# Optimization experiments

Hardware: AMD Instinct MI355X
Metric: run time of the kernel (lower is better)

The kernel has to match this reference:

```python
import jax, jax.numpy as jnp
import numpy as np

N_NODES = 20000
N_EDGES = 320000
DIM_IN = 768
DIM_H = 512
S_HOPS = 3
NUM_GNNS = 4
NEG_SLOPE = 0.2  # DGL GATConv default


def setup_inputs() -> dict:
    key = jax.random.key(0)
    ks = jax.random.split(key, 12)
    feat = jax.random.normal(ks[0], (N_NODES, DIM_IN), dtype=jnp.float32)
    src = jax.random.randint(ks[1], (N_EDGES,), 0, N_NODES)
    dst = jax.random.randint(ks[2], (N_EDGES,), 0, N_NODES)
    # learned params
    fc_W = jax.random.normal(ks[3], (DIM_IN, DIM_H), dtype=jnp.float32) * 0.02
    fc_b = jnp.zeros((DIM_H,), dtype=jnp.float32)
    gat_W = jax.random.normal(ks[4], (NUM_GNNS, DIM_H, DIM_H), dtype=jnp.float32) * 0.02
    gat_al = jax.random.normal(ks[5], (NUM_GNNS, DIM_H), dtype=jnp.float32) * 0.1
    gat_ar = jax.random.normal(ks[6], (NUM_GNNS, DIM_H), dtype=jnp.float32) * 0.1
    gat_b = jnp.zeros((NUM_GNNS, DIM_H), dtype=jnp.float32)
    beta = jnp.ones((S_HOPS + 1,), dtype=jnp.float32)
    return {"feat": feat, "fc_W": fc_W, "fc_b": fc_b, "gat_W": gat_W,
            "gat_al": gat_al, "gat_ar": gat_ar, "gat_b": gat_b,
            "beta": beta, "src": src, "dst": dst}


def _gat_layer(h, W, a_l, a_r, b, src, dst):
    z = h @ W                                   # [N, DH]
    el = z @ a_l                                # [N]
    er = z @ a_r                                # [N]
    e = jax.nn.leaky_relu(el[src] + er[dst], NEG_SLOPE)  # [E]
    # edge softmax over incoming edges of each dst node
    m = jax.ops.segment_max(e, dst, num_segments=N_NODES)
    ex = jnp.exp(e - m[dst])
    denom = jax.ops.segment_sum(ex, dst, num_segments=N_NODES)
    alpha = ex / denom[dst]                     # [E]
    out = jax.ops.segment_sum(alpha[:, None] * z[src], dst, num_segments=N_NODES)
    return out + b


def reference(feat, fc_W, fc_b, gat_W, gat_al, gat_ar, gat_b, beta, src, dst):
    h = feat @ fc_W + fc_b                      # dim_in -> 512
    for l in range(NUM_GNNS):
        h = _gat_layer(h, gat_W[l], gat_al[l], gat_ar[l], gat_b[l], src, dst)
    # A_hat = A + I propagation; A_hat @ Z = scatter(Z[src] -> dst) + Z
    Z_prev = h
    Z = beta[0] * Z_prev                        # accumulated Z is computed but the
    for s in range(1, S_HOPS + 1):              # original module returns Z_prev
        Z_s = jax.ops.segment_sum(Z_prev[src], dst, num_segments=N_NODES) + Z_prev
        Z = Z + beta[s] * Z_s
        Z_prev = Z_s
    return Z_prev
```

## Files before the change

kernel.cpp:

```cpp
#include <hip/hip_runtime.h>
#include <math.h>

#define N_NODES 20000
#define M_PAD   20096
#define N_EDGES 320000
#define DIM_IN 768
#define DIM_H 512
#define NUM_GNNS 4
#define NEG_SLOPE 0.2f

typedef __attribute__((ext_vector_type(8))) short short8;
typedef __attribute__((ext_vector_type(4))) float f32x4;

#define GPTR(p) (const __attribute__((address_space(1))) void*)(p)
#define LPTR(p) (__attribute__((address_space(3))) void*)(p)

__device__ __forceinline__ float bf2f(unsigned int lo16) {
  return __uint_as_float(lo16 << 16);
}
__device__ __forceinline__ unsigned short f2bf(float f) {
  unsigned int u = __float_as_uint(f);
  u += 0x7FFFu + ((u >> 16) & 1u);
  return (unsigned short)(u >> 16);
}
__device__ __forceinline__ void unpack8(uint4 v, float* f) {
  f[0] = bf2f(v.x & 0xffffu); f[1] = bf2f(v.x >> 16);
  f[2] = bf2f(v.y & 0xffffu); f[3] = bf2f(v.y >> 16);
  f[4] = bf2f(v.z & 0xffffu); f[5] = bf2f(v.z >> 16);
  f[6] = bf2f(v.w & 0xffffu); f[7] = bf2f(v.w >> 16);
}
__device__ __forceinline__ uint4 pack8(const float* o) {
  uint4 pv;
  pv.x = (unsigned)f2bf(o[0]) | ((unsigned)f2bf(o[1]) << 16);
  pv.y = (unsigned)f2bf(o[2]) | ((unsigned)f2bf(o[3]) << 16);
  pv.z = (unsigned)f2bf(o[4]) | ((unsigned)f2bf(o[5]) << 16);
  pv.w = (unsigned)f2bf(o[6]) | ((unsigned)f2bf(o[7]) << 16);
  return pv;
}

__device__ __forceinline__ float waveReduceSum(float v) {
#pragma unroll
  for (int off = 32; off > 0; off >>= 1) v += __shfl_xor(v, off, 64);
  return v;
}
__device__ __forceinline__ float waveReduceMax(float v) {
#pragma unroll
  for (int off = 32; off > 0; off >>= 1) v = fmaxf(v, __shfl_xor(v, off, 64));
  return v;
}

__global__ __launch_bounds__(256) void gemm_mfma_bf16(
    const unsigned short* __restrict__ A,
    const unsigned short* __restrict__ Bt,
    const float* __restrict__ bias,
    unsigned short* __restrict__ Cbf,
    int K) {
  __shared__ __align__(16) unsigned short As[128 * 32];
  __shared__ __align__(16) unsigned short Bs[128 * 32];
  int tid = threadIdx.x;
  int wave = tid >> 6, lane = tid & 63;
  int wm = wave >> 1, wn = wave & 1;

  int rl = lane >> 2;
  int kc = (lane & 3) ^ ((lane >> 3) & 3);
  int r0 = 32 * wave;
  const unsigned short* gA0 = A + (size_t)(blockIdx.y * 128 + r0 + rl) * K + kc * 8;
  const unsigned short* gA1 = gA0 + (size_t)16 * K;
  const unsigned short* gB0 = Bt + (size_t)(blockIdx.x * 128 + r0 + rl) * K + kc * 8;
  const unsigned short* gB1 = gB0 + (size_t)16 * K;
  unsigned short* lA0 = As + r0 * 32;
  unsigned short* lA1 = As + (r0 + 16) * 32;
  unsigned short* lB0 = Bs + r0 * 32;
  unsigned short* lB1 = Bs + (r0 + 16) * 32;

  int mrow = lane & 15;
  int q = lane >> 4;
  int swz = (q ^ ((mrow >> 1) & 3)) * 8;
  const short8* ra = (const short8*)(As + (64 * wm + mrow) * 32 + swz);
  const short8* rb = (const short8*)(Bs + (64 * wn + mrow) * 32 + swz);

  f32x4 acc[4][4];
#pragma unroll
  for (int i = 0; i < 4; ++i)
#pragma unroll
    for (int j = 0; j < 4; ++j) acc[i][j] = (f32x4)(0.f);

  for (int k0 = 0; k0 < K; k0 += 32) {
    __syncthreads();
    __builtin_amdgcn_global_load_lds(GPTR(gA0 + k0), LPTR(lA0), 16, 0, 0);
    __builtin_amdgcn_global_load_lds(GPTR(gA1 + k0), LPTR(lA1), 16, 0, 0);
    __builtin_amdgcn_global_load_lds(GPTR(gB0 + k0), LPTR(lB0), 16, 0, 0);
    __builtin_amdgcn_global_load_lds(GPTR(gB1 + k0), LPTR(lB1), 16, 0, 0);
    __syncthreads();
    short8 a[4], b[4];
#pragma unroll
    for (int t = 0; t < 4; ++t) a[t] = ra[t * 64];
#pragma unroll
    for (int t = 0; t < 4; ++t) b[t] = rb[t * 64];
#pragma unroll
    for (int mt = 0; mt < 4; ++mt)
#pragma unroll
      for (int nt = 0; nt < 4; ++nt)
        acc[mt][nt] = __builtin_amdgcn_mfma_f32_16x16x32_bf16(a[mt], b[nt], acc[mt][nt], 0, 0, 0);
  }

  int colb = blockIdx.x * 128 + 64 * wn + (lane & 15);
  int rowb = blockIdx.y * 128 + 64 * wm + 4 * q;
#pragma unroll
  for (int nt = 0; nt < 4; ++nt) {
    int col = colb + 16 * nt;
    float bv = bias ? bias[col] : 0.f;
#pragma unroll
    for (int mt = 0; mt < 4; ++mt) {
      int row = rowb + 16 * mt;
#pragma unroll
      for (int i = 0; i < 4; ++i)
        Cbf[(size_t)(row + i) * DIM_H + col] = f2bf(acc[mt][nt][i] + bv);
    }
  }
}

__global__ void convert_feat(const float* __restrict__ feat, unsigned short* __restrict__ Abf) {
  int t = blockIdx.x * blockDim.x + threadIdx.x;
  const int CHUNKS = M_PAD * DIM_IN / 8;
  if (t >= CHUNKS) return;
  int row = t / (DIM_IN / 8);
  uint4 o;
  if (row < N_NODES) {
    const float4* p = (const float4*)(feat + (size_t)t * 8);
    float4 x = p[0], y = p[1];
    o.x = (unsigned)f2bf(x.x) | ((unsigned)f2bf(x.y) << 16);
    o.y = (unsigned)f2bf(x.z) | ((unsigned)f2bf(x.w) << 16);
    o.z = (unsigned)f2bf(y.x) | ((unsigned)f2bf(y.y) << 16);
    o.w = (unsigned)f2bf(y.z) | ((unsigned)f2bf(y.w) << 16);
  } else {
    o = make_uint4(0, 0, 0, 0);
  }
  ((uint4*)Abf)[t] = o;
}

__global__ void transpose_bf16(const float* __restrict__ in, unsigned short* __restrict__ out,
                               int R, int C) {
  int r = blockIdx.x * blockDim.x + threadIdx.x;
  int c = blockIdx.y;
  size_t base = (size_t)blockIdx.z * R * C;
  if (r < R) out[base + (size_t)c * R + r] = f2bf(in[base + (size_t)r * C + c]);
}

__global__ void count_edges(const int* __restrict__ dst, int* __restrict__ counts) {
  int k = blockIdx.x * blockDim.x + threadIdx.x;
  if (k < N_EDGES) atomicAdd(&counts[dst[k]], 1);
}

__global__ __launch_bounds__(1024) void scan_kernel(const int* __restrict__ counts,
                                                    int* __restrict__ indptr) {
  __shared__ int part[1024];
  int tid = threadIdx.x;
  const int CH = (N_NODES + 1023) / 1024;
  int base = tid * CH;
  int s = 0;
  for (int i = 0; i < CH; ++i) {
    int idx = base + i;
    if (idx < N_NODES) s += counts[idx];
  }
  part[tid] = s;
  __syncthreads();
  for (int off = 1; off < 1024; off <<= 1) {
    int v = (tid >= off) ? part[tid - off] : 0;
    __syncthreads();
    part[tid] += v;
    __syncthreads();
  }
  int run = (tid == 0) ? 0 : part[tid - 1];
  for (int i = 0; i < CH; ++i) {
    int idx = base + i;
    if (idx < N_NODES) {
      indptr[idx] = run;
      run += counts[idx];
      if (idx == N_NODES - 1) indptr[N_NODES] = run;
    }
  }
}

__global__ void fill_adj(const int* __restrict__ src, const int* __restrict__ dst,
                         const int* __restrict__ indptr, int* __restrict__ cursor,
                         int* __restrict__ adjsrc) {
  int k = blockIdx.x * blockDim.x + threadIdx.x;
  if (k < N_EDGES) {
    int d = dst[k];
    int pos = atomicAdd(&cursor[d], 1);
    adjsrc[indptr[d] + pos] = src[k];
  }
}

__global__ __launch_bounds__(256) void eler_bf(const unsigned short* __restrict__ zbf,
                                               const float* __restrict__ al,
                                               const float* __restrict__ ar,
                                               float* __restrict__ el, float* __restrict__ er) {
  int wid = (blockIdx.x * blockDim.x + threadIdx.x) >> 6;
  int lane = threadIdx.x & 63;
  if (wid >= N_NODES) return;
  uint4 zv = ((const uint4*)(zbf + (size_t)wid * DIM_H))[lane];
  float z[8];
  unpack8(zv, z);
  const float4* al4 = (const float4*)(al + lane * 8);
  const float4* ar4 = (const float4*)(ar + lane * 8);
  float4 a0 = al4[0], a1 = al4[1], r0 = ar4[0], r1 = ar4[1];
  float sl = z[0] * a0.x + z[1] * a0.y + z[2] * a0.z + z[3] * a0.w +
             z[4] * a1.x + z[5] * a1.y + z[6] * a1.z + z[7] * a1.w;
  float sr = z[0] * r0.x + z[1] * r0.y + z[2] * r0.z + z[3] * r0.w +
             z[4] * r1.x + z[5] * r1.y + z[6] * r1.z + z[7] * r1.w;
  sl = waveReduceSum(sl);
  sr = waveReduceSum(sr);
  if (lane == 0) { el[wid] = sl; er[wid] = sr; }
}

__global__ __launch_bounds__(256) void gat_aggregate_bf(
    const unsigned short* __restrict__ zbf, const float* __restrict__ el,
    const float* __restrict__ er, const int* __restrict__ indptr,
    const int* __restrict__ adjsrc, const float* __restrict__ bias,
    unsigned short* __restrict__ out_bf) {
  int v = (blockIdx.x * blockDim.x + threadIdx.x) >> 6;
  int lane = threadIdx.x & 63;
  if (v >= N_NODES) return;
  int begin = indptr[v], end = indptr[v + 1];
  float er_v = er[v];

  float m = -INFINITY;
  for (int j = begin + lane; j < end; j += 64) {
    float e = el[adjsrc[j]] + er_v;
    e = (e >= 0.f) ? e : NEG_SLOPE * e;
    m = fmaxf(m, e);
  }
  m = waveReduceMax(m);

  float ssum = 0.f;
  for (int j = begin + lane; j < end; j += 64) {
    float e = el[adjsrc[j]] + er_v;
    e = (e >= 0.f) ? e : NEG_SLOPE * e;
    ssum += __expf(e - m);
  }
  float denom = waveReduceSum(ssum);
  float inv = (end > begin) ? 1.f / denom : 0.f;

  float acc[8] = {};
  for (int c = begin; c < end; c += 64) {
    int cc = min(64, end - c);
    int has = (c + lane < end);
    int sIdx = has ? adjsrc[c + lane] : 0;
    float e = has ? el[sIdx] + er_v : 0.f;
    e = (e >= 0.f) ? e : NEG_SLOPE * e;
    float wl = has ? __expf(e - m) * inv : 0.f;
    int t = 0;
    for (; t + 4 <= cc; t += 4) {
      int s0 = __shfl(sIdx, t + 0), s1 = __shfl(sIdx, t + 1);
      int s2 = __shfl(sIdx, t + 2), s3 = __shfl(sIdx, t + 3);
      float w0 = __shfl(wl, t + 0), w1 = __shfl(wl, t + 1);
      float w2 = __shfl(wl, t + 2), w3 = __shfl(wl, t + 3);
      uint4 z0 = ((const uint4*)(zbf + (size_t)s0 * DIM_H))[lane];
      uint4 z1 = ((const uint4*)(zbf + (size_t)s1 * DIM_H))[lane];
      uint4 z2 = ((const uint4*)(zbf + (size_t)s2 * DIM_H))[lane];
      uint4 z3 = ((const uint4*)(zbf + (size_t)s3 * DIM_H))[lane];
      float f0[8], f1[8], f2[8], f3[8];
      unpack8(z0, f0); unpack8(z1, f1); unpack8(z2, f2); unpack8(z3, f3);
#pragma unroll
      for (int i = 0; i < 8; ++i)
        acc[i] += w0 * f0[i] + w1 * f1[i] + w2 * f2[i] + w3 * f3[i];
    }
    for (; t < cc; ++t) {
      int s0 = __shfl(sIdx, t);
      float w0 = __shfl(wl, t);
      uint4 z0 = ((const uint4*)(zbf + (size_t)s0 * DIM_H))[lane];
      float f0[8];
      unpack8(z0, f0);
#pragma unroll
      for (int i = 0; i < 8; ++i) acc[i] += w0 * f0[i];
    }
  }
  const float4* b4 = (const float4*)(bias + lane * 8);
  float4 b0 = b4[0], b1 = b4[1];
  float o[8] = {acc[0] + b0.x, acc[1] + b0.y, acc[2] + b0.z, acc[3] + b0.w,
                acc[4] + b1.x, acc[5] + b1.y, acc[6] + b1.z, acc[7] + b1.w};
  ((uint4*)(out_bf + (size_t)v * DIM_H))[lane] = pack8(o);
}

__global__ __launch_bounds__(256) void propagate_bf(const unsigned short* __restrict__ zin,
                                                    const int* __restrict__ indptr,
                                                    const int* __restrict__ adjsrc,
                                                    unsigned short* __restrict__ out_bf,
                                                    float* __restrict__ out_f32) {
  int v = (blockIdx.x * blockDim.x + threadIdx.x) >> 6;
  int lane = threadIdx.x & 63;
  if (v >= N_NODES) return;
  uint4 sv = ((const uint4*)(zin + (size_t)v * DIM_H))[lane];
  float acc[8];
  unpack8(sv, acc);
  int begin = indptr[v], end = indptr[v + 1];
  for (int c = begin; c < end; c += 64) {
    int cc = min(64, end - c);
    int sIdx = (c + lane < end) ? adjsrc[c + lane] : 0;
    int t = 0;
    for (; t + 4 <= cc; t += 4) {
      int s0 = __shfl(sIdx, t + 0), s1 = __shfl(sIdx, t + 1);
      int s2 = __shfl(sIdx, t + 2), s3 = __shfl(sIdx, t + 3);
      uint4 z0 = ((const uint4*)(zin + (size_t)s0 * DIM_H))[lane];
      uint4 z1 = ((const uint4*)(zin + (size_t)s1 * DIM_H))[lane];
      uint4 z2 = ((const uint4*)(zin + (size_t)s2 * DIM_H))[lane];
      uint4 z3 = ((const uint4*)(zin + (size_t)s3 * DIM_H))[lane];
      float f0[8], f1[8], f2[8], f3[8];
      unpack8(z0, f0); unpack8(z1, f1); unpack8(z2, f2); unpack8(z3, f3);
#pragma unroll
      for (int i = 0; i < 8; ++i) acc[i] += f0[i] + f1[i] + f2[i] + f3[i];
    }
    for (; t < cc; ++t) {
      int s0 = __shfl(sIdx, t);
      uint4 z0 = ((const uint4*)(zin + (size_t)s0 * DIM_H))[lane];
      float f0[8];
      unpack8(z0, f0);
#pragma unroll
      for (int i = 0; i < 8; ++i) acc[i] += f0[i];
    }
  }
  if (out_bf) {
    ((uint4*)(out_bf + (size_t)v * DIM_H))[lane] = pack8(acc);
  } else {
    float4* fr = (float4*)(out_f32 + (size_t)v * DIM_H + lane * 8);
    fr[0] = make_float4(acc[0], acc[1], acc[2], acc[3]);
    fr[1] = make_float4(acc[4], acc[5], acc[6], acc[7]);
  }
}

extern "C" void kernel_launch(void* const* d_in, const int* in_sizes, int n_in,
                              void* d_out, int out_size, void* d_ws, size_t ws_size,
                              hipStream_t stream) {
  const float* feat = (const float*)d_in[0];
  const float* fc_W = (const float*)d_in[1];
  const float* fc_b = (const float*)d_in[2];
  const float* gat_W = (const float*)d_in[3];
  const float* gat_al = (const float*)d_in[4];
  const float* gat_ar = (const float*)d_in[5];
  const float* gat_b = (const float*)d_in[6];
  const int* src = (const int*)d_in[8];
  const int* dst = (const int*)d_in[9];
  float* out = (float*)d_out;

  char* w = (char*)d_ws;
  auto alloc = [&](size_t bytes) {
    char* p = w;
    w += (bytes + 255) & ~(size_t)255;
    return p;
  };
  unsigned short* hbf   = (unsigned short*)alloc((size_t)M_PAD * DIM_H * 2);
  unsigned short* fcWt  = (unsigned short*)alloc((size_t)DIM_H * DIM_IN * 2);
  unsigned short* gatWt = (unsigned short*)alloc((size_t)NUM_GNNS * DIM_H * DIM_H * 2);
  float* el    = (float*)alloc((size_t)N_NODES * 4);
  float* er    = (float*)alloc((size_t)N_NODES * 4);
  int* counts  = (int*)alloc((size_t)2 * N_NODES * 4);
  int* cursor  = counts + N_NODES;
  int* indptr  = (int*)alloc((size_t)(N_NODES + 1) * 4);
  int* adjsrc  = (int*)alloc((size_t)N_EDGES * 4);
  char* uni = alloc((size_t)M_PAD * DIM_IN * 2);
  unsigned short* Abf = (unsigned short*)uni;
  unsigned short* Z1  = (unsigned short*)uni;
  unsigned short* zbf = (unsigned short*)d_out;

  hipMemsetAsync(counts, 0, sizeof(int) * 2 * N_NODES, stream);
  count_edges<<<(N_EDGES + 255) / 256, 256, 0, stream>>>(dst, counts);
  scan_kernel<<<1, 1024, 0, stream>>>(counts, indptr);
  fill_adj<<<(N_EDGES + 255) / 256, 256, 0, stream>>>(src, dst, indptr, cursor, adjsrc);

  convert_feat<<<(M_PAD * DIM_IN / 8 + 255) / 256, 256, 0, stream>>>(feat, Abf);
  transpose_bf16<<<dim3((DIM_IN + 255) / 256, DIM_H, 1), 256, 0, stream>>>(fc_W, fcWt, DIM_IN, DIM_H);
  transpose_bf16<<<dim3((DIM_H + 255) / 256, DIM_H, NUM_GNNS), 256, 0, stream>>>(gat_W, gatWt, DIM_H, DIM_H);

  dim3 ggrid(DIM_H / 128, M_PAD / 128);

  gemm_mfma_bf16<<<ggrid, 256, 0, stream>>>(Abf, fcWt, fc_b, hbf, DIM_IN);

  int nwaveblocks = (N_NODES * 64 + 255) / 256;
  for (int l = 0; l < NUM_GNNS; ++l) {
    gemm_mfma_bf16<<<ggrid, 256, 0, stream>>>(hbf, gatWt + (size_t)l * DIM_H * DIM_H,
                                              nullptr, zbf, DIM_H);
    eler_bf<<<nwaveblocks, 256, 0, stream>>>(zbf, gat_al + (size_t)l * DIM_H,
                                             gat_ar + (size_t)l * DIM_H, el, er);
    gat_aggregate_bf<<<nwaveblocks, 256, 0, stream>>>(
        zbf, el, er, indptr, adjsrc, gat_b + (size_t)l * DIM_H, hbf);
  }

  propagate_bf<<<nwaveblocks, 256, 0, stream>>>(hbf, indptr, adjsrc, Z1, nullptr);
  propagate_bf<<<nwaveblocks, 256, 0, stream>>>(Z1, indptr, adjsrc, hbf, nullptr);
  propagate_bf<<<nwaveblocks, 256, 0, stream>>>(hbf, indptr, adjsrc, nullptr, out);
}
```

Before: 656.3 us.

## Fuse attention logits into GEMM epilogue, use online softmax, deepen gather unroll

Computes el/er inside the GAT GEMM epilogue from fp32 accumulators, using shuffle reductions and atomicAdd into zeroed buffers, which removes the separate eler kernel and its re-read of z. Merges the max pass and the sum pass of the edge softmax into a single online-softmax pass. Adds an 8-way unrolled gather in the aggregate and propagate kernels so more row loads are in flight. The trade-offs are a memset per layer, float atomics whose accumulation order is not deterministic, and higher register pressure from the wider unroll.

```diff
diff --git a/kernel.cpp b/kernel.cpp
--- a/kernel.cpp
+++ b/kernel.cpp
@@ -8,6 +8,7 @@
 #define DIM_H 512
 #define NUM_GNNS 4
 #define NEG_SLOPE 0.2f
+#define NEG_HUGE -3.0e38f
 
 typedef __attribute__((ext_vector_type(8))) short short8;
 typedef __attribute__((ext_vector_type(4))) float f32x4;
@@ -38,23 +39,14 @@
   return pv;
 }
 
-__device__ __forceinline__ float waveReduceSum(float v) {
-#pragma unroll
-  for (int off = 32; off > 0; off >>= 1) v += __shfl_xor(v, off, 64);
-  return v;
-}
-__device__ __forceinline__ float waveReduceMax(float v) {
-#pragma unroll
-  for (int off = 32; off > 0; off >>= 1) v = fmaxf(v, __shfl_xor(v, off, 64));
-  return v;
-}
-
 __global__ __launch_bounds__(256) void gemm_mfma_bf16(
     const unsigned short* __restrict__ A,
     const unsigned short* __restrict__ Bt,
     const float* __restrict__ bias,
     unsigned short* __restrict__ Cbf,
-    int K) {
+    int K,
+    const float* __restrict__ al, const float* __restrict__ ar,
+    float* __restrict__ el, float* __restrict__ er) {
   __shared__ __align__(16) unsigned short As[128 * 32];
   __shared__ __align__(16) unsigned short Bs[128 * 32];
   int tid = threadIdx.x;
@@ -106,6 +98,7 @@
 
   int colb = blockIdx.x * 128 + 64 * wn + (lane & 15);
   int rowb = blockIdx.y * 128 + 64 * wm + 4 * q;
+
 #pragma unroll
   for (int nt = 0; nt < 4; ++nt) {
     int col = colb + 16 * nt;
@@ -116,6 +109,35 @@
 #pragma unroll
       for (int i = 0; i < 4; ++i)
         Cbf[(size_t)(row + i) * DIM_H + col] = f2bf(acc[mt][nt][i] + bv);
+    }
+  }
+
+  if (al) {
+    float alv[4], arv[4];
+#pragma unroll
+    for (int nt = 0; nt < 4; ++nt) {
+      alv[nt] = al[colb + 16 * nt];
+      arv[nt] = ar[colb + 16 * nt];
+    }
+#pragma unroll
+    for (int mt = 0; mt < 4; ++mt) {
+#pragma unroll
+      for (int i = 0; i < 4; ++i) {
+        float pl = acc[mt][0][i] * alv[0] + acc[mt][1][i] * alv[1] +
+                   acc[mt][2][i] * alv[2] + acc[mt][3][i] * alv[3];
+        float pr = acc[mt][0][i] * arv[0] + acc[mt][1][i] * arv[1] +
+                   acc[mt][2][i] * arv[2] + acc[mt][3][i] * arv[3];
+#pragma unroll
+        for (int msk = 1; msk < 16; msk <<= 1) {
+          pl += __shfl_xor(pl, msk, 64);
+          pr += __shfl_xor(pr, msk, 64);
+        }
+        if ((lane & 15) == 0) {
+          int row = rowb + 16 * mt + i;
+          atomicAdd(&el[row], pl);
+          atomicAdd(&er[row], pr);
+        }
+      }
     }
   }
 }
@@ -193,28 +215,6 @@
   }
 }
 
-__global__ __launch_bounds__(256) void eler_bf(const unsigned short* __restrict__ zbf,
-                                               const float* __restrict__ al,
-                                               const float* __restrict__ ar,
-                                               float* __restrict__ el, float* __restrict__ er) {
-  int wid = (blockIdx.x * blockDim.x + threadIdx.x) >> 6;
-  int lane = threadIdx.x & 63;
-  if (wid >= N_NODES) return;
-  uint4 zv = ((const uint4*)(zbf + (size_t)wid * DIM_H))[lane];
-  float z[8];
-  unpack8(zv, z);
-  const float4* al4 = (const float4*)(al + lane * 8);
-  const float4* ar4 = (const float4*)(ar + lane * 8);
-  float4 a0 = al4[0], a1 = al4[1], r0 = ar4[0], r1 = ar4[1];
-  float sl = z[0] * a0.x + z[1] * a0.y + z[2] * a0.z + z[3] * a0.w +
-             z[4] * a1.x + z[5] * a1.y + z[6] * a1.z + z[7] * a1.w;
-  float sr = z[0] * r0.x + z[1] * r0.y + z[2] * r0.z + z[3] * r0.w +
-             z[4] * r1.x + z[5] * r1.y + z[6] * r1.z + z[7] * r1.w;
-  sl = waveReduceSum(sl);
-  sr = waveReduceSum(sr);
-  if (lane == 0) { el[wid] = sl; er[wid] = sr; }
-}
-
 __global__ __launch_bounds__(256) void gat_aggregate_bf(
     const unsigned short* __restrict__ zbf, const float* __restrict__ el,
     const float* __restrict__ er, const int* __restrict__ indptr,
@@ -226,22 +226,23 @@
   int begin = indptr[v], end = indptr[v + 1];
   float er_v = er[v];
 
-  float m = -INFINITY;
+  float m = NEG_HUGE, ssum = 0.f;
   for (int j = begin + lane; j < end; j += 64) {
     float e = el[adjsrc[j]] + er_v;
     e = (e >= 0.f) ? e : NEG_SLOPE * e;
-    m = fmaxf(m, e);
-  }
-  m = waveReduceMax(m);
-
-  float ssum = 0.f;
-  for (int j = begin + lane; j < end; j += 64) {
-    float e = el[adjsrc[j]] + er_v;
-    e = (e >= 0.f) ? e : NEG_SLOPE * e;
-    ssum += __expf(e - m);
-  }
-  float denom = waveReduceSum(ssum);
-  float inv = (end > begin) ? 1.f / denom : 0.f;
+    float nm = fmaxf(m, e);
+    ssum = ssum * __expf(m - nm) + __expf(e - nm);
+    m = nm;
+  }
+#pragma unroll
+  for (int off = 32; off > 0; off >>= 1) {
+    float om = __shfl_xor(m, off, 64);
+    float os = __shfl_xor(ssum, off, 64);
+    float nm = fmaxf(m, om);
+    ssum = ssum * __expf(m - nm) + os * __expf(om - nm);
+    m = nm;
+  }
+  float inv = (end > begin) ? 1.f / ssum : 0.f;
 
   float acc[8] = {};
   for (int c = begin; c < end; c += 64) {
@@ -252,20 +253,39 @@
     e = (e >= 0.f) ? e : NEG_SLOPE * e;
     float wl = has ? __expf(e - m) * inv : 0.f;
     int t = 0;
+    for (; t + 8 <= cc; t += 8) {
+      uint4 z[8];
+      float w[8];
+#pragma unroll
+      for (int u = 0; u < 8; ++u) {
+        int s = __shfl(sIdx, t + u);
+        w[u] = __shfl(wl, t + u);
+        z[u] = ((const uint4*)(zbf + (size_t)s * DIM_H))[lane];
+      }
+#pragma unroll
+      for (int u = 0; u < 8; ++u) {
+        float f[8];
+        unpack8(z[u], f);
+#pragma unroll
+        for (int i = 0; i < 8; ++i) acc[i] += w[u] * f[i];
+      }
+    }
     for (; t + 4 <= cc; t += 4) {
-      int s0 = __shfl(sIdx, t + 0), s1 = __shfl(sIdx, t + 1);
-      int s2 = __shfl(sIdx, t + 2), s3 = __shfl(sIdx, t + 3);
-      float w0 = __shfl(wl, t + 0), w1 = __shfl(wl, t + 1);
-      float w2 = __shfl(wl, t + 2), w3 = __shfl(wl, t + 3);
-      uint4 z0 = ((const uint4*)(zbf + (size_t)s0 * DIM_H))[lane];
-      uint4 z1 = ((const uint4*)(zbf + (size_t)s1 * DIM_H))[lane];
-      uint4 z2 = ((const uint4*)(zbf + (size_t)s2 * DIM_H))[lane];
-      uint4 z3 = ((const uint4*)(zbf + (size_t)s3 * DIM_H))[lane];
-      float f0[8], f1[8], f2[8], f3[8];
-      unpack8(z0, f0); unpack8(z1, f1); unpack8(z2, f2); unpack8(z3, f3);
-#pragma unroll
-      for (int i = 0; i < 8; ++i)
-        acc[i] += w0 * f0[i] + w1 * f1[i] + w2 * f2[i] + w3 * f3[i];
+      uint4 z[4];
+      float w[4];
+#pragma unroll
+      for (int u = 0; u < 4; ++u) {
+        int s = __shfl(sIdx, t + u);
+        w[u] = __shfl(wl, t + u);
+        z[u] = ((const uint4*)(zbf + (size_t)s * DIM_H))[lane];
+      }
+#pragma unroll
+      for (int u = 0; u < 4; ++u) {
+        float f[8];
+        unpack8(z[u], f);
+#pragma unroll
+        for (int i = 0; i < 8; ++i) acc[i] += w[u] * f[i];
+      }
     }
     for (; t < cc; ++t) {
       int s0 = __shfl(sIdx, t);
@@ -300,17 +320,35 @@
     int cc = min(64, end - c);
     int sIdx = (c + lane < end) ? adjsrc[c + lane] : 0;
     int t = 0;
+    for (; t + 8 <= cc; t += 8) {
+      uint4 z[8];
+#pragma unroll
+      for (int u = 0; u < 8; ++u) {
+        int s = __shfl(sIdx, t + u);
+        z[u] = ((const uint4*)(zin + (size_t)s * DIM_H))[lane];
+      }
+#pragma unroll
+      for (int u = 0; u < 8; ++u) {
+        float f[8];
+        unpack8(z[u], f);
+#pragma unroll
+        for (int i = 0; i < 8; ++i) acc[i] += f[i];
+      }
+    }
     for (; t + 4 <= cc; t += 4) {
-      int s0 = __shfl(sIdx, t + 0), s1 = __shfl(sIdx, t + 1);
-      int s2 = __shfl(sIdx, t + 2), s3 = __shfl(sIdx, t + 3);
-      uint4 z0 = ((const uint4*)(zin + (size_t)s0 * DIM_H))[lane];
-      uint4 z1 = ((const uint4*)(zin + (size_t)s1 * DIM_H))[lane];
-      uint4 z2 = ((const uint4*)(zin + (size_t)s2 * DIM_H))[lane];
-      uint4 z3 = ((const uint4*)(zin + (size_t)s3 * DIM_H))[lane];
-      float f0[8], f1[8], f2[8], f3[8];
-      unpack8(z0, f0); unpack8(z1, f1); unpack8(z2, f2); unpack8(z3, f3);
-#pragma unroll
-      for (int i = 0; i < 8; ++i) acc[i] += f0[i] + f1[i] + f2[i] + f3[i];
+      uint4 z[4];
+#pragma unroll
+      for (int u = 0; u < 4; ++u) {
+        int s = __shfl(sIdx, t + u);
+        z[u] = ((const uint4*)(zin + (size_t)s * DIM_H))[lane];
+      }
+#pragma unroll
+      for (int u = 0; u < 4; ++u) {
+        float f[8];
+        unpack8(z[u], f);
+#pragma unroll
+        for (int i = 0; i < 8; ++i) acc[i] += f[i];
+      }
     }
     for (; t < cc; ++t) {
       int s0 = __shfl(sIdx, t);
@@ -353,8 +391,8 @@
   unsigned short* hbf   = (unsigned short*)alloc((size_t)M_PAD * DIM_H * 2);
   unsigned short* fcWt  = (unsigned short*)alloc((size_t)DIM_H * DIM_IN * 2);
   unsigned short* gatWt = (unsigned short*)alloc((size_t)NUM_GNNS * DIM_H * DIM_H * 2);
-  float* el    = (float*)alloc((size_t)N_NODES * 4);
-  float* er    = (float*)alloc((size_t)N_NODES * 4);
+  float* el    = (float*)alloc((size_t)2 * M_PAD * 4);
+  float* er    = el + M_PAD;
   int* counts  = (int*)alloc((size_t)2 * N_NODES * 4);
   int* cursor  = counts + N_NODES;
   int* indptr  = (int*)alloc((size_t)(N_NODES + 1) * 4);
@@ -375,14 +413,16 @@
 
   dim3 ggrid(DIM_H / 128, M_PAD / 128);
 
-  gemm_mfma_bf16<<<ggrid, 256, 0, stream>>>(Abf, fcWt, fc_b, hbf, DIM_IN);
+  gemm_mfma_bf16<<<ggrid, 256, 0, stream>>>(Abf, fcWt, fc_b, hbf, DIM_IN,
+                                            nullptr, nullptr, nullptr, nullptr);
 
   int nwaveblocks = (N_NODES * 64 + 255) / 256;
   for (int l = 0; l < NUM_GNNS; ++l) {
+    hipMemsetAsync(el, 0, sizeof(float) * 2 * M_PAD, stream);
     gemm_mfma_bf16<<<ggrid, 256, 0, stream>>>(hbf, gatWt + (size_t)l * DIM_H * DIM_H,
-                                              nullptr, zbf, DIM_H);
-    eler_bf<<<nwaveblocks, 256, 0, stream>>>(zbf, gat_al + (size_t)l * DIM_H,
-                                             gat_ar + (size_t)l * DIM_H, el, er);
+                                              nullptr, zbf, DIM_H,
+                                              gat_al + (size_t)l * DIM_H,
+                                              gat_ar + (size_t)l * DIM_H, el, er);
     gat_aggregate_bf<<<nwaveblocks, 256, 0, stream>>>(
         zbf, el, er, indptr, adjsrc, gat_b + (size_t)l * DIM_H, hbf);
   }
```

Measured after the change: 704.5 us. +7.4%, slower.
